# Optimization experiments

Hardware: AMD Instinct MI355X
Metric: run time of the kernel (lower is better)

## Reference

```python
import jax, jax.numpy as jnp
import numpy as np
from jax import lax

N, H, W = 16, 112, 112
CIN, COUT, K = 256, 256, 3
STRIDE, PAD = 1, 1


def setup_inputs() -> dict:
    key = jax.random.key(0)
    kx, kw = jax.random.split(key)
    # int8-valued activations and weights, stored as int32 for portable integer conv
    x = jax.random.randint(kx, (N, H, W, CIN), -128, 128, dtype=jnp.int32)
    # weight layout matches the torch module: (out_channels, kH, kW, in_channels) == OHWI
    weight = jax.random.randint(kw, (COUT, K, K, CIN), -128, 128, dtype=jnp.int32)
    return {"x": x, "weight": weight}


def reference(x, weight):
    y = lax.conv_general_dilated(
        x,
        weight,
        window_strides=(STRIDE, STRIDE),
        padding=[(PAD, PAD), (PAD, PAD)],
        dimension_numbers=("NHWC", "OHWI", "NHWC"),
        preferred_element_type=jnp.int32,
    )
    return y  # (N, H, W, COUT) int32
```

## Files before the change

kernel.cpp:

```cpp
#include <hip/hip_runtime.h>
#include <stdint.h>

#define NN   16
#define HH   112
#define WW   112
#define CIN  256
#define COUT 256
#define HP   114
#define WP   114
#define M_TOTAL (NN * HH * WW)
#define XP_BYTES ((size_t)NN * HP * WP * CIN)
#define WPK_BYTES ((size_t)9 * COUT * CIN)

typedef int v4i __attribute__((ext_vector_type(4)));

__device__ __forceinline__ void load_lds16(const void* g, void* l) {
  __builtin_amdgcn_global_load_lds(
      (const __attribute__((address_space(1))) void*)g,
      (__attribute__((address_space(3))) void*)l, 16, 0, 0);
}

__device__ __forceinline__ int pack4(int a, int b, int c, int d) {
  return (a & 255) | ((b & 255) << 8) | ((c & 255) << 16) | (d << 24);
}

__global__ void pack_x_kernel(const int* __restrict__ x, char* __restrict__ xp) {
  int t = blockIdx.x * 256 + threadIdx.x;
  int g = t & 15;
  int p = t >> 4;
  int w = p % WW;
  int t2 = p / WW;
  int h = t2 % HH;
  int n = t2 / HH;
  const int* src = x + (size_t)p * CIN + g * 16;
  int4 i0 = ((const int4*)src)[0];
  int4 i1 = ((const int4*)src)[1];
  int4 i2 = ((const int4*)src)[2];
  int4 i3 = ((const int4*)src)[3];
  int4 ov = make_int4(pack4(i0.x, i0.y, i0.z, i0.w),
                      pack4(i1.x, i1.y, i1.z, i1.w),
                      pack4(i2.x, i2.y, i2.z, i2.w),
                      pack4(i3.x, i3.y, i3.z, i3.w));
  size_t dst = (((size_t)n * HP + (h + 1)) * WP + (w + 1)) * CIN + (size_t)g * 16;
  *(int4*)(xp + dst) = ov;
}

__global__ void zero_border_kernel(char* __restrict__ xp) {
  int t = blockIdx.x * 256 + threadIdx.x;
  int g = t & 15;
  int pix = t >> 4;
  int n = pix / 452;
  int b = pix % 452;
  int h, w;
  if (b < 114) { h = 0; w = b; }
  else if (b < 228) { h = 113; w = b - 114; }
  else { int r = b - 228; h = 1 + (r >> 1); w = (r & 1) ? 113 : 0; }
  size_t dst = (((size_t)n * HP + h) * WP + w) * CIN + (size_t)g * 16;
  *(int4*)(xp + dst) = make_int4(0, 0, 0, 0);
}

__global__ void pack_w_kernel(const int* __restrict__ wgt, char* __restrict__ wp) {
  int t = blockIdx.x * 256 + threadIdx.x;
  int g = t & 15;
  int r = t >> 4;
  int tap = r % 9;
  int cout = r / 9;
  const int* src = wgt + ((size_t)(cout * 9 + tap)) * CIN + g * 16;
  int4 i0 = ((const int4*)src)[0];
  int4 i1 = ((const int4*)src)[1];
  int4 i2 = ((const int4*)src)[2];
  int4 i3 = ((const int4*)src)[3];
  int4 ov = make_int4(pack4(i0.x, i0.y, i0.z, i0.w),
                      pack4(i1.x, i1.y, i1.z, i1.w),
                      pack4(i2.x, i2.y, i2.z, i2.w),
                      pack4(i3.x, i3.y, i3.z, i3.w));
  size_t dst = ((size_t)tap * COUT + cout) * CIN + (size_t)g * 16;
  *(int4*)(wp + dst) = ov;
}

__global__ __launch_bounds__(256, 2) void conv_mfma_kernel(const char* __restrict__ xp,
                                                           const char* __restrict__ wp,
                                                           int* __restrict__ out) {
  __shared__ __align__(16) char As[128 * 64];
  __shared__ __align__(16) char Bs[256 * 64];
  const int tid = threadIdx.x;
  const int lane = tid & 63;
  const int wave = tid >> 6;
  const int mtile = blockIdx.x;

  const char* gptr[6];
  char* lptr[6];
  int  isA[6];
#pragma unroll
  for (int j = 0; j < 6; j++) {
    int c = wave * 6 + j;
    if (c < 8) {
      int row = c * 16 + (lane >> 2);
      int colg = (lane & 3) ^ ((row >> 1) & 3);
      int m = mtile * 128 + row;
      int w = m % WW;
      int t2 = m / WW;
      int h = t2 % HH;
      int n = t2 / HH;
      gptr[j] = xp + (((size_t)n * HP + h) * WP + w) * CIN + (size_t)colg * 16;
      lptr[j] = As + c * 1024;
      isA[j] = 1;
    } else {
      int cb = c - 8;
      int row = cb * 16 + (lane >> 2);
      int colg = (lane & 3) ^ ((row >> 1) & 3);
      gptr[j] = wp + (size_t)row * CIN + (size_t)colg * 16;
      lptr[j] = Bs + cb * 1024;
      isA[j] = 0;
    }
  }

  const int wm = wave & 1;
  const int wn = wave >> 1;
  int aoff[4], boff[8];
#pragma unroll
  for (int i = 0; i < 4; i++) {
    int ra = wm * 64 + i * 16 + (lane & 15);
    aoff[i] = ra * 64 + (((lane >> 4) ^ ((ra >> 1) & 3)) * 16);
  }
#pragma unroll
  for (int j = 0; j < 8; j++) {
    int rb = wn * 128 + j * 16 + (lane & 15);
    boff[j] = rb * 64 + (((lane >> 4) ^ ((rb >> 1) & 3)) * 16);
  }

  v4i acc[4][8];
#pragma unroll
  for (int i = 0; i < 4; i++)
#pragma unroll
    for (int j = 0; j < 8; j++) acc[i][j] = (v4i){0, 0, 0, 0};

#pragma unroll 1
  for (int ks = 0; ks < 36; ks++) {
    const int tap = ks >> 2;
    const int kb = ks & 3;
    const int ky = tap / 3;
    const int kx = tap - ky * 3;
    const int offA = (ky * WP + kx) * CIN + kb * 64;
    const int offB = tap * (COUT * CIN) + kb * 64;
    __syncthreads();
#pragma unroll
    for (int j = 0; j < 6; j++)
      load_lds16(gptr[j] + (isA[j] ? offA : offB), lptr[j]);
    __syncthreads();
    v4i af[4], bf[8];
#pragma unroll
    for (int i = 0; i < 4; i++) af[i] = *(const v4i*)(As + aoff[i]);
#pragma unroll
    for (int j = 0; j < 8; j++) bf[j] = *(const v4i*)(Bs + boff[j]);
#pragma unroll
    for (int i = 0; i < 4; i++)
#pragma unroll
      for (int j = 0; j < 8; j++)
        acc[i][j] = __builtin_amdgcn_mfma_i32_16x16x64_i8(af[i], bf[j], acc[i][j], 0, 0, 0);
  }

#pragma unroll
  for (int i = 0; i < 4; i++) {
    const int mg = mtile * 128 + wm * 64 + i * 16 + ((lane >> 4) * 4);
#pragma unroll
    for (int r = 0; r < 4; r++) {
      int* orow = out + (size_t)(mg + r) * COUT + wn * 128 + (lane & 15);
#pragma unroll
      for (int j = 0; j < 8; j++) orow[j * 16] = acc[i][j][r];
    }
  }
}

__global__ void conv_naive_kernel(const int* __restrict__ x, const int* __restrict__ wgt,
                                  int* __restrict__ out, int total) {
  int idx = blockIdx.x * 256 + threadIdx.x;
  if (idx >= total) return;
  int co = idx & 255;
  int p = idx >> 8;
  int w = p % WW;
  int t2 = p / WW;
  int h = t2 % HH;
  int n = t2 / HH;
  int acc = 0;
  for (int ky = 0; ky < 3; ky++) {
    int ih = h + ky - 1;
    if (ih < 0 || ih >= HH) continue;
    for (int kx = 0; kx < 3; kx++) {
      int iw = w + kx - 1;
      if (iw < 0 || iw >= WW) continue;
      const int* xs = x + (((size_t)n * HH + ih) * WW + iw) * CIN;
      const int* ws = wgt + ((size_t)co * 9 + ky * 3 + kx) * CIN;
      for (int ci = 0; ci < CIN; ci++) acc += xs[ci] * ws[ci];
    }
  }
  out[idx] = acc;
}

extern "C" void kernel_launch(void* const* d_in, const int* in_sizes, int n_in,
                              void* d_out, int out_size, void* d_ws, size_t ws_size,
                              hipStream_t stream) {
  const int* x = (const int*)d_in[0];
  const int* wgt = (const int*)d_in[1];
  int* out = (int*)d_out;
  const size_t need = XP_BYTES + WPK_BYTES;
  if (ws_size >= need) {
    char* xp = (char*)d_ws;
    char* wp = xp + XP_BYTES;
    pack_x_kernel<<<(M_TOTAL * 16) / 256, 256, 0, stream>>>(x, xp);
    zero_border_kernel<<<(7232 * 16) / 256, 256, 0, stream>>>(xp);
    pack_w_kernel<<<(2304 * 16) / 256, 256, 0, stream>>>(wgt, wp);
    conv_mfma_kernel<<<M_TOTAL / 128, 256, 0, stream>>>(xp, wp, out);
  } else {
    conv_naive_kernel<<<(out_size + 255) / 256, 256, 0, stream>>>(x, wgt, out, out_size);
  }
}
```

Baseline: 481.4 us.

## Double-buffer LDS stages in int8 conv and coalesce pack kernels

The MFMA conv kernel now keeps two LDS buffers for the A and B tiles. It issues the global-to-LDS load for the next K step before computing on the current one, so each step needs one barrier instead of two. The goal is to overlap memory traffic with MFMA work, at the cost of doubling LDS use to 48KB per block. Separately, the x and weight pack kernels now have each thread convert four consecutive int32 values, so global reads are fully coalesced instead of using 64-byte strided chunks per thread. The overlap only pays off if the compiler does not insert a full vmcnt wait before the LDS reads.

```diff
diff --git a/kernel.cpp b/kernel.cpp
--- a/kernel.cpp
+++ b/kernel.cpp
@@ -26,23 +26,16 @@
 
 __global__ void pack_x_kernel(const int* __restrict__ x, char* __restrict__ xp) {
   int t = blockIdx.x * 256 + threadIdx.x;
-  int g = t & 15;
-  int p = t >> 4;
+  int c4 = t & 63;
+  int p = t >> 6;
   int w = p % WW;
   int t2 = p / WW;
   int h = t2 % HH;
   int n = t2 / HH;
-  const int* src = x + (size_t)p * CIN + g * 16;
-  int4 i0 = ((const int4*)src)[0];
-  int4 i1 = ((const int4*)src)[1];
-  int4 i2 = ((const int4*)src)[2];
-  int4 i3 = ((const int4*)src)[3];
-  int4 ov = make_int4(pack4(i0.x, i0.y, i0.z, i0.w),
-                      pack4(i1.x, i1.y, i1.z, i1.w),
-                      pack4(i2.x, i2.y, i2.z, i2.w),
-                      pack4(i3.x, i3.y, i3.z, i3.w));
-  size_t dst = (((size_t)n * HP + (h + 1)) * WP + (w + 1)) * CIN + (size_t)g * 16;
-  *(int4*)(xp + dst) = ov;
+  int4 v = *(const int4*)(x + (size_t)t * 4);
+  int ov = pack4(v.x, v.y, v.z, v.w);
+  size_t dst = (((size_t)n * HP + (h + 1)) * WP + (w + 1)) * CIN + (size_t)c4 * 4;
+  *(int*)(xp + dst) = ov;
 }
 
 __global__ void zero_border_kernel(char* __restrict__ xp) {
@@ -61,28 +54,21 @@
 
 __global__ void pack_w_kernel(const int* __restrict__ wgt, char* __restrict__ wp) {
   int t = blockIdx.x * 256 + threadIdx.x;
-  int g = t & 15;
-  int r = t >> 4;
+  int c4 = t & 63;
+  int r = t >> 6;
   int tap = r % 9;
   int cout = r / 9;
-  const int* src = wgt + ((size_t)(cout * 9 + tap)) * CIN + g * 16;
-  int4 i0 = ((const int4*)src)[0];
-  int4 i1 = ((const int4*)src)[1];
-  int4 i2 = ((const int4*)src)[2];
-  int4 i3 = ((const int4*)src)[3];
-  int4 ov = make_int4(pack4(i0.x, i0.y, i0.z, i0.w),
-                      pack4(i1.x, i1.y, i1.z, i1.w),
-                      pack4(i2.x, i2.y, i2.z, i2.w),
-                      pack4(i3.x, i3.y, i3.z, i3.w));
-  size_t dst = ((size_t)tap * COUT + cout) * CIN + (size_t)g * 16;
-  *(int4*)(wp + dst) = ov;
+  int4 v = *(const int4*)(wgt + (size_t)t * 4);
+  int ov = pack4(v.x, v.y, v.z, v.w);
+  size_t dst = ((size_t)tap * COUT + cout) * CIN + (size_t)c4 * 4;
+  *(int*)(wp + dst) = ov;
 }
 
 __global__ __launch_bounds__(256, 2) void conv_mfma_kernel(const char* __restrict__ xp,
                                                            const char* __restrict__ wp,
                                                            int* __restrict__ out) {
-  __shared__ __align__(16) char As[128 * 64];
-  __shared__ __align__(16) char Bs[256 * 64];
+  __shared__ __align__(16) char As[2 * 128 * 64];
+  __shared__ __align__(16) char Bs[2 * 256 * 64];
   const int tid = threadIdx.x;
   const int lane = tid & 63;
   const int wave = tid >> 6;
@@ -135,24 +121,33 @@
 #pragma unroll
     for (int j = 0; j < 8; j++) acc[i][j] = (v4i){0, 0, 0, 0};
 
+  auto stage = [&](int ks, int b) {
+    int tap = ks >> 2;
+    int kb = ks & 3;
+    int ky = tap / 3;
+    int kx = tap - ky * 3;
+    int offA = (ky * WP + kx) * CIN + kb * 64;
+    int offB = tap * (COUT * CIN) + kb * 64;
+#pragma unroll
+    for (int j = 0; j < 6; j++)
+      load_lds16(gptr[j] + (isA[j] ? offA : offB),
+                 lptr[j] + (isA[j] ? b * 8192 : b * 16384));
+  };
+
+  stage(0, 0);
+
 #pragma unroll 1
   for (int ks = 0; ks < 36; ks++) {
-    const int tap = ks >> 2;
-    const int kb = ks & 3;
-    const int ky = tap / 3;
-    const int kx = tap - ky * 3;
-    const int offA = (ky * WP + kx) * CIN + kb * 64;
-    const int offB = tap * (COUT * CIN) + kb * 64;
+    const int cur = ks & 1;
     __syncthreads();
-#pragma unroll
-    for (int j = 0; j < 6; j++)
-      load_lds16(gptr[j] + (isA[j] ? offA : offB), lptr[j]);
-    __syncthreads();
+    if (ks + 1 < 36) stage(ks + 1, cur ^ 1);
+    const char* Ab = As + cur * 8192;
+    const char* Bb = Bs + cur * 16384;
     v4i af[4], bf[8];
 #pragma unroll
-    for (int i = 0; i < 4; i++) af[i] = *(const v4i*)(As + aoff[i]);
-#pragma unroll
-    for (int j = 0; j < 8; j++) bf[j] = *(const v4i*)(Bs + boff[j]);
+    for (int i = 0; i < 4; i++) af[i] = *(const v4i*)(Ab + aoff[i]);
+#pragma unroll
+    for (int j = 0; j < 8; j++) bf[j] = *(const v4i*)(Bb + boff[j]);
 #pragma unroll
     for (int i = 0; i < 4; i++)
 #pragma unroll
@@ -207,9 +202,9 @@
   if (ws_size >= need) {
     char* xp = (char*)d_ws;
     char* wp = xp + XP_BYTES;
-    pack_x_kernel<<<(M_TOTAL * 16) / 256, 256, 0, stream>>>(x, xp);
+    pack_x_kernel<<<(M_TOTAL * 64) / 256, 256, 0, stream>>>(x, xp);
     zero_border_kernel<<<(7232 * 16) / 256, 256, 0, stream>>>(xp);
-    pack_w_kernel<<<(2304 * 16) / 256, 256, 0, stream>>>(wgt, wp);
+    pack_w_kernel<<<(2304 * 64) / 256, 256, 0, stream>>>(wgt, wp);
     conv_mfma_kernel<<<M_TOTAL / 128, 256, 0, stream>>>(xp, wp, out);
   } else {
     conv_naive_kernel<<<(out_size + 255) / 256, 256, 0, stream>>>(x, wgt, out, out_size);
```

Result: faster. 460.7 us (-4.3%).
